# Optimization experiments

Measured on AMD Instinct MI355X. Metric: run time of the kernel, lower is better.

The kernel has to match this reference:

```python
import jax, jax.numpy as jnp
import numpy as np

DIM = 1024
D_STATE = 16
EXPAND = 2
D_CONV = 4
D_INNER = DIM * EXPAND          # 2048
DT_RANK = (DIM + 15) // 16      # ceil(dim/16) = 64
BATCH = 2
SEQ = 1024


def setup_inputs() -> dict:
    key = jax.random.key(0)
    ks = jax.random.split(key, 8)
    s = 0.02
    A = jnp.broadcast_to(jnp.arange(1, D_STATE + 1, dtype=jnp.float32), (D_INNER, D_STATE))
    return {
        "x": jax.random.normal(ks[0], (BATCH, SEQ, DIM), jnp.float32),
        "in_w": jax.random.normal(ks[1], (2 * D_INNER, DIM), jnp.float32) * s,
        "conv_w": jax.random.normal(ks[2], (D_INNER, 1, D_CONV), jnp.float32) * s,   # depthwise conv kernel (OIH)
        "conv_b": jnp.zeros((D_INNER,), jnp.float32),
        "xproj_w": jax.random.normal(ks[3], (DT_RANK + 2 * D_STATE, D_INNER), jnp.float32) * s,
        "dt_w": jax.random.normal(ks[4], (D_INNER, DT_RANK), jnp.float32) * s,
        "dt_b": jax.random.normal(ks[5], (D_INNER,), jnp.float32) * s,
        "A_log": jnp.log(A),
        "D": jnp.ones((D_INNER,), jnp.float32),
        "out_w": jax.random.normal(ks[6], (DIM, D_INNER), jnp.float32) * s,
    }


def _selective_scan(u, delta, A, B, C, D):
    # u: (b, d_in, l); delta: (b, l, d_in); A: (d_in, n); B, C: (b, l, n); D: (d_in,)
    dA = jnp.exp(jnp.einsum('bld,dn->lbdn', delta, A))          # (l, b, d_in, n)
    dBu = jnp.einsum('bld,bln,bdl->lbdn', delta, B, u)          # (l, b, d_in, n)
    Ct = jnp.transpose(C, (1, 0, 2))                            # (l, b, n)

    def step(carry, inp):
        a, bu, c = inp
        carry = a * carry + bu                                  # (b, d_in, n)
        y = jnp.einsum('bdn,bn->bd', carry, c)
        return carry, y

    x0 = jnp.zeros(dA.shape[1:], dA.dtype)
    _, ys = jax.lax.scan(step, x0, (dA, dBu, Ct))               # ys: (l, b, d_in)
    y = jnp.transpose(ys, (1, 2, 0))                            # (b, d_in, l)
    return y + u * D[:, None]


def reference(x, in_w, conv_w, conv_b, xproj_w, dt_w, dt_b, A_log, D, out_w):
    b, l, d = x.shape
    xr = x @ in_w.T                                             # (b, l, 2*d_in)
    xx, res = jnp.split(xr, 2, axis=-1)
    xx = jnp.transpose(xx, (0, 2, 1))                           # (b, d_in, l)
    # causal depthwise conv: left-pad d_conv-1 == torch pad=d_conv-1 then [:, :, :l]
    xx = jax.lax.conv_general_dilated(
        xx, conv_w, window_strides=(1,), padding=[(D_CONV - 1, 0)],
        dimension_numbers=('NCH', 'OIH', 'NCH'), feature_group_count=D_INNER
    ) + conv_b[None, :, None]
    xx = jax.nn.silu(xx)
    A = -jnp.exp(A_log)
    x_dbl = jnp.einsum('bdl,kd->blk', xx, xproj_w)              # (b, l, dt_rank + 2n)
    delta, B, C = jnp.split(x_dbl, [DT_RANK, DT_RANK + D_STATE], axis=-1)
    delta = jax.nn.softplus(delta @ dt_w.T + dt_b)              # (b, l, d_in)
    y = _selective_scan(xx, delta, A, B, C, D)                  # (b, d_in, l)
    y = y * jax.nn.silu(jnp.transpose(res, (0, 2, 1)))
    return jnp.transpose(y, (0, 2, 1)) @ out_w.T                # (b, l, dim)
```

## Files before the change

### kernel.cpp

```cpp
#include <hip/hip_runtime.h>
#include <hip/hip_bf16.h>
#include <stdint.h>

#define DIM      1024
#define D_STATE  16
#define D_CONV   4
#define D_INNER  2048
#define DT_RANK  64
#define BATCH    2
#define SEQ      1024
#define MROWS    (BATCH * SEQ)
#define NPROJ    (2 * D_INNER)
#define XDBL_K   (DT_RANK + 2 * D_STATE)

#define LC       16
#define NC       (SEQ / LC)
#define SLANES   (BATCH * D_INNER * D_STATE)

typedef __attribute__((ext_vector_type(8))) short short8;
typedef __attribute__((ext_vector_type(4))) float f32x4;
typedef unsigned short ushort_t;

__device__ __forceinline__ unsigned short f2bf(float f) {
    __hip_bfloat16 b = __float2bfloat16(f);
    return *reinterpret_cast<unsigned short*>(&b);
}
__device__ __forceinline__ float bf2f(unsigned short u) {
    __hip_bfloat16 b;
    *reinterpret_cast<unsigned short*>(&b) = u;
    return __bfloat162float(b);
}

__device__ __forceinline__ void gload_lds16(const unsigned short* g, unsigned short* l) {
    __builtin_amdgcn_global_load_lds(
        (const __attribute__((address_space(1))) void*)g,
        (__attribute__((address_space(3))) void*)l,
        16, 0, 0);
}

#define SG0 524288
#define SG1 1048576
#define SG2 65536
#define SG3 524288
#define SPLIT_GRANULES (SG0 + SG1 + SG2 + SG3)

__global__ __launch_bounds__(256) void split_all(
    const float* __restrict__ x,   const float* __restrict__ in_w,
    const float* __restrict__ xpw, const float* __restrict__ ow,
    ushort_t* __restrict__ xh,   ushort_t* __restrict__ xl,
    ushort_t* __restrict__ iwh,  ushort_t* __restrict__ xph,
    ushort_t* __restrict__ owh)
{
    int g = blockIdx.x * 256 + threadIdx.x;
    const float* src; int K, rows_src; ushort_t *dh, *dl; bool lo;
    if (g < SG0)               { src = x;    K = 1024; rows_src = 2048; dh = xh;  dl = xl; lo = true;  }
    else if ((g -= SG0) < SG1) { src = in_w; K = 1024; rows_src = 4096; dh = iwh; dl = 0;  lo = false; }
    else if ((g -= SG1) < SG2) { src = xpw;  K = 2048; rows_src = 96;   dh = xph; dl = 0;  lo = false; }
    else                       { g -= SG2;   src = ow; K = 2048; rows_src = 1024; dh = owh; dl = 0; lo = false; }

    const int kq = K >> 2;
    const int r = g / kq;
    const int k4 = (g - r * kq) << 2;
    float4 v = make_float4(0.f, 0.f, 0.f, 0.f);
    if (r < rows_src)
        v = *reinterpret_cast<const float4*>(src + (size_t)r * K + k4);
    const unsigned short h0 = f2bf(v.x), h1 = f2bf(v.y), h2 = f2bf(v.z), h3 = f2bf(v.w);
    *reinterpret_cast<ushort4*>(dh + (size_t)r * K + k4) = make_ushort4(h0, h1, h2, h3);
    if (lo) {
        const unsigned short l0 = f2bf(v.x - bf2f(h0)), l1 = f2bf(v.y - bf2f(h1));
        const unsigned short l2 = f2bf(v.z - bf2f(h2)), l3 = f2bf(v.w - bf2f(h3));
        *reinterpret_cast<ushort4*>(dl + (size_t)r * K + k4) = make_ushort4(l0, l1, l2, l3);
    }
}

__device__ __forceinline__ short8 frag_ld(const unsigned short* base, int row, int slot) {
    const char* p = reinterpret_cast<const char*>(base) +
                    row * 128 + (((slot ^ (row & 7)) & 7) << 4);
    return *reinterpret_cast<const short8*>(p);
}

template <int EPI>
__global__ __launch_bounds__(256) void gemm_bf2(
    const ushort_t* __restrict__ Ahg, const ushort_t* __restrict__ Alg, int lda,
    const ushort_t* __restrict__ Bhg, int ldb,
    float* __restrict__ C, int ldc, size_t czstride,
    const float* __restrict__ bias, int kLen)
{
    __shared__ ushort_t Ahs[128 * 64];
    __shared__ ushort_t Als[128 * 64];
    __shared__ ushort_t Bhs[128 * 64];

    const int tid = threadIdx.x;
    const int lane = tid & 63;
    const int w = tid >> 6;
    const int wr = w >> 1, wc = w & 1;
    const int fr = lane & 15, fg = lane >> 4;
    const int m0 = blockIdx.y * 128;
    const int n0 = blockIdx.x * 128;
    const int kOff = blockIdx.z * kLen;
    Ahg += kOff; Alg += kOff; Bhg += kOff;
    C += (size_t)blockIdx.z * czstride;

    f32x4 zero = {0.f, 0.f, 0.f, 0.f};
    f32x4 acc[4][4];
#pragma unroll
    for (int i = 0; i < 4; ++i)
#pragma unroll
        for (int j = 0; j < 4; ++j) acc[i][j] = zero;

    for (int k0 = 0; k0 < kLen; k0 += 64) {
#pragma unroll
        for (int it = 0; it < 4; ++it) {
            const int f = it * 256 + tid;
            const int row = f >> 3;
            const int gc = ((f & 7) ^ (row & 7)) << 3;
            const size_t ga = (size_t)(m0 + row) * lda + k0 + gc;
            const size_t gb = (size_t)(n0 + row) * ldb + k0 + gc;
            gload_lds16(Ahg + ga, &Ahs[f * 8]);
            gload_lds16(Alg + ga, &Als[f * 8]);
            gload_lds16(Bhg + gb, &Bhs[f * 8]);
        }
        __syncthreads();

#pragma unroll
        for (int kk = 0; kk < 2; ++kk) {
            short8 ah[4], bh[4], al[4];
#pragma unroll
            for (int i = 0; i < 4; ++i) {
                ah[i] = frag_ld(Ahs, wr * 64 + i * 16 + fr, kk * 4 + fg);
                bh[i] = frag_ld(Bhs, wc * 64 + i * 16 + fr, kk * 4 + fg);
            }
#pragma unroll
            for (int i = 0; i < 4; ++i)
#pragma unroll
                for (int j = 0; j < 4; ++j)
                    acc[i][j] = __builtin_amdgcn_mfma_f32_16x16x32_bf16(
                        ah[i], bh[j], acc[i][j], 0, 0, 0);
#pragma unroll
            for (int i = 0; i < 4; ++i)
                al[i] = frag_ld(Als, wr * 64 + i * 16 + fr, kk * 4 + fg);
#pragma unroll
            for (int i = 0; i < 4; ++i)
#pragma unroll
                for (int j = 0; j < 4; ++j)
                    acc[i][j] = __builtin_amdgcn_mfma_f32_16x16x32_bf16(
                        al[i], bh[j], acc[i][j], 0, 0, 0);
        }
        __syncthreads();
    }

#pragma unroll
    for (int i = 0; i < 4; ++i) {
        const int mrow = m0 + wr * 64 + i * 16 + fg * 4;
#pragma unroll
        for (int j = 0; j < 4; ++j) {
            const int col = n0 + wc * 64 + j * 16 + fr;
#pragma unroll
            for (int r = 0; r < 4; ++r) {
                float v = acc[i][j][r];
                if constexpr (EPI == 1) {
                    v += bias[col];
                    v = (v > 20.f) ? v : log1pf(__expf(v));
                }
                C[(size_t)(mrow + r) * ldc + col] = v;
            }
        }
    }
}

#define DTC 64
#define DTR 64
__global__ __launch_bounds__(256) void dt_softplus(
    const float* __restrict__ XDBL, const float* __restrict__ dtw,
    const float* __restrict__ dtb, float* __restrict__ DELTA)
{
    __shared__ float X[DTR][68];

    const int tid = threadIdx.x;
    const int lane = tid & 63;
    const int wv = tid >> 6;
    const int d = blockIdx.x * DTC + lane;
    const int m0 = blockIdx.y * DTR;

#pragma unroll
    for (int i = 0; i < 4; ++i) {
        const int g = tid + i * 256;
        const int r = g >> 4;
        const int q4 = (g & 15) << 2;
        const float4 v = *reinterpret_cast<const float4*>(
            XDBL + (size_t)(m0 + r) * XDBL_K + q4);
        *reinterpret_cast<float4*>(&X[r][q4]) = v;
    }

    float wreg[DT_RANK];
#pragma unroll
    for (int k4 = 0; k4 < DT_RANK / 4; ++k4) {
        const float4 v = *reinterpret_cast<const float4*>(
            dtw + (size_t)d * DT_RANK + k4 * 4);
        wreg[k4 * 4 + 0] = v.x;
        wreg[k4 * 4 + 1] = v.y;
        wreg[k4 * 4 + 2] = v.z;
        wreg[k4 * 4 + 3] = v.w;
    }
    const float bias = dtb[d];
    __syncthreads();

#pragma unroll
    for (int r = 0; r < DTR / 4; ++r) {
        const int rl = wv * (DTR / 4) + r;
        float a0 = bias, a1 = 0.f, a2 = 0.f, a3 = 0.f;
#pragma unroll
        for (int k = 0; k < DT_RANK; k += 4) {
            const float4 xv = *reinterpret_cast<const float4*>(&X[rl][k]);
            a0 = fmaf(xv.x, wreg[k + 0], a0);
            a1 = fmaf(xv.y, wreg[k + 1], a1);
            a2 = fmaf(xv.z, wreg[k + 2], a2);
            a3 = fmaf(xv.w, wreg[k + 3], a3);
        }
        float acc = (a0 + a1) + (a2 + a3);
        acc = (acc > 20.f) ? acc : log1pf(__expf(acc));
        DELTA[(size_t)(m0 + rl) * D_INNER + d] = acc;
    }
}

__global__ __launch_bounds__(256) void conv_silu(
    const float* __restrict__ XR, const float* __restrict__ cw,
    const float* __restrict__ cb, ushort_t* __restrict__ Uh,
    ushort_t* __restrict__ Ul)
{
    const int idx = blockIdx.x * 256 + threadIdx.x;
    const int d = idx & (D_INNER - 1);
    const int m = idx >> 11;
    const int l = m & (SEQ - 1);

    float acc = cb[d];
#pragma unroll
    for (int j = 0; j < D_CONV; ++j) {
        const int ll = l - (D_CONV - 1) + j;
        if (ll >= 0)
            acc = fmaf(XR[(size_t)(m - (D_CONV - 1) + j) * NPROJ + d],
                       cw[d * D_CONV + j], acc);
    }
    const float s = acc / (1.f + __expf(-acc));
    const unsigned short h = f2bf(s);
    Uh[idx] = h;
    Ul[idx] = f2bf(s - bf2f(h));
}

__global__ __launch_bounds__(256) void scan_phase1(
    const float* __restrict__ DELTA, const ushort_t* __restrict__ Uh,
    const ushort_t* __restrict__ Ul, const float* __restrict__ XDBL,
    const float* __restrict__ A_log, float* __restrict__ P,
    float* __restrict__ HL)
{
    const int tid = threadIdx.x;
    const int d = blockIdx.x * 256 + tid;
    const int c = blockIdx.y;
    const int b = blockIdx.z;

    float a[16];
#pragma unroll
    for (int q = 0; q < 4; ++q) {
        const float4 v = *reinterpret_cast<const float4*>(A_log + (size_t)d * 16 + q * 4);
        a[q * 4 + 0] = -__expf(v.x);
        a[q * 4 + 1] = -__expf(v.y);
        a[q * 4 + 2] = -__expf(v.z);
        a[q * 4 + 3] = -__expf(v.w);
    }
    float h[16];
#pragma unroll
    for (int n = 0; n < 16; ++n) h[n] = 0.f;
    float sd = 0.f;
    const size_t base = (size_t)b * SEQ + (size_t)c * LC;

#pragma unroll 4
    for (int t = 0; t < LC; ++t) {
        const size_t m = base + t;
        const float delta = DELTA[m * D_INNER + d];
        const float u = bf2f(Uh[m * D_INNER + d]) + bf2f(Ul[m * D_INNER + d]);
        const float du = delta * u;
        const float* xb = XDBL + m * XDBL_K + DT_RANK;
        float bv[16];
#pragma unroll
        for (int n = 0; n < 16; ++n) bv[n] = xb[n];
        sd += delta;
#pragma unroll
        for (int n = 0; n < 16; ++n) {
            const float dA = __expf(delta * a[n]);
            h[n] = fmaf(dA, h[n], du * bv[n]);
        }
    }

    const size_t idx = (size_t)c * SLANES + ((size_t)b * D_INNER + d) * 16;
#pragma unroll
    for (int q = 0; q < 4; ++q) {
        float4 pv, hv;
        pv.x = __expf(a[q * 4 + 0] * sd);
        pv.y = __expf(a[q * 4 + 1] * sd);
        pv.z = __expf(a[q * 4 + 2] * sd);
        pv.w = __expf(a[q * 4 + 3] * sd);
        hv.x = h[q * 4 + 0]; hv.y = h[q * 4 + 1];
        hv.z = h[q * 4 + 2]; hv.w = h[q * 4 + 3];
        *reinterpret_cast<float4*>(&P[idx + q * 4]) = pv;
        *reinterpret_cast<float4*>(&HL[idx + q * 4]) = hv;
    }
}

__global__ __launch_bounds__(256) void scan_phase2(
    float* __restrict__ P, const float* __restrict__ HL)
{
    const int t = blockIdx.x * 256 + threadIdx.x;
    float h = 0.f;
#pragma unroll 8
    for (int c = 0; c < NC; ++c) {
        const size_t idx = (size_t)c * SLANES + t;
        const float p = P[idx];
        const float hl = HL[idx];
        P[idx] = h;
        h = fmaf(p, h, hl);
    }
}

__global__ __launch_bounds__(256) void scan_phase3(
    const float* __restrict__ DELTA, const ushort_t* __restrict__ Uh,
    const ushort_t* __restrict__ Ul, const float* __restrict__ XDBL,
    const float* __restrict__ XR, const float* __restrict__ A_log,
    const float* __restrict__ Dp, const float* __restrict__ H0,
    ushort_t* __restrict__ Yh, ushort_t* __restrict__ Yl)
{
    const int tid = threadIdx.x;
    const int d = blockIdx.x * 256 + tid;
    const int c = blockIdx.y;
    const int b = blockIdx.z;

    float a[16];
#pragma unroll
    for (int q = 0; q < 4; ++q) {
        const float4 v = *reinterpret_cast<const float4*>(A_log + (size_t)d * 16 + q * 4);
        a[q * 4 + 0] = -__expf(v.x);
        a[q * 4 + 1] = -__expf(v.y);
        a[q * 4 + 2] = -__expf(v.z);
        a[q * 4 + 3] = -__expf(v.w);
    }
    const float Dd = Dp[d];

    float h[16];
    const size_t idx0 = (size_t)c * SLANES + ((size_t)b * D_INNER + d) * 16;
#pragma unroll
    for (int q = 0; q < 4; ++q) {
        const float4 v = *reinterpret_cast<const float4*>(&H0[idx0 + q * 4]);
        h[q * 4 + 0] = v.x; h[q * 4 + 1] = v.y;
        h[q * 4 + 2] = v.z; h[q * 4 + 3] = v.w;
    }
    const size_t base = (size_t)b * SEQ + (size_t)c * LC;

#pragma unroll 4
    for (int t = 0; t < LC; ++t) {
        const size_t m = base + t;
        const float delta = DELTA[m * D_INNER + d];
        const float u = bf2f(Uh[m * D_INNER + d]) + bf2f(Ul[m * D_INNER + d]);
        const float du = delta * u;
        const float* xb = XDBL + m * XDBL_K + DT_RANK;
        float bv[16], cv[16];
#pragma unroll
        for (int n = 0; n < 16; ++n) bv[n] = xb[n];
#pragma unroll
        for (int n = 0; n < 16; ++n) cv[n] = xb[16 + n];

        float y0 = 0.f, y1 = 0.f, y2 = 0.f, y3 = 0.f;
#pragma unroll
        for (int n = 0; n < 4; ++n) {
            const float dA0 = __expf(delta * a[n]);
            const float dA1 = __expf(delta * a[n + 4]);
            const float dA2 = __expf(delta * a[n + 8]);
            const float dA3 = __expf(delta * a[n + 12]);
            h[n]      = fmaf(dA0, h[n],      du * bv[n]);
            h[n + 4]  = fmaf(dA1, h[n + 4],  du * bv[n + 4]);
            h[n + 8]  = fmaf(dA2, h[n + 8],  du * bv[n + 8]);
            h[n + 12] = fmaf(dA3, h[n + 12], du * bv[n + 12]);
            y0 = fmaf(h[n],      cv[n],      y0);
            y1 = fmaf(h[n + 4],  cv[n + 4],  y1);
            y2 = fmaf(h[n + 8],  cv[n + 8],  y2);
            y3 = fmaf(h[n + 12], cv[n + 12], y3);
        }
        const float y = (y0 + y1) + (y2 + y3) + u * Dd;
        const float r = XR[m * NPROJ + D_INNER + d];
        const float sr = r / (1.f + __expf(-r));
        const float yg = y * sr;
        const unsigned short hh = f2bf(yg);
        Yh[m * D_INNER + d] = hh;
        Yl[m * D_INNER + d] = f2bf(yg - bf2f(hh));
    }
}

__global__ __launch_bounds__(256) void reduce_xdbl(
    const float* __restrict__ PP, float* __restrict__ XDBL)
{
    const int t = blockIdx.x * 256 + threadIdx.x;
    const int m = t / XDBL_K;
    const int n = t - m * XDBL_K;
    float s = 0.f;
#pragma unroll
    for (int z = 0; z < 16; ++z)
        s += PP[(size_t)z * MROWS * 128 + (size_t)m * 128 + n];
    XDBL[t] = s;
}

__global__ __launch_bounds__(256) void reduce_out(
    const float* __restrict__ OP, float* __restrict__ out)
{
    const int t = blockIdx.x * 256 + threadIdx.x;
    float4 s = *reinterpret_cast<const float4*>(OP + (size_t)t * 4);
#pragma unroll
    for (int z = 1; z < 4; ++z) {
        const float4 v = *reinterpret_cast<const float4*>(
            OP + (size_t)z * MROWS * DIM + (size_t)t * 4);
        s.x += v.x; s.y += v.y; s.z += v.z; s.w += v.w;
    }
    *reinterpret_cast<float4*>(out + (size_t)t * 4) = s;
}

extern "C" void kernel_launch(void* const* d_in, const int* in_sizes, int n_in,
                              void* d_out, int out_size, void* d_ws, size_t ws_size,
                              hipStream_t stream)
{
    const float* x       = (const float*)d_in[0];
    const float* in_w    = (const float*)d_in[1];
    const float* conv_w  = (const float*)d_in[2];
    const float* conv_b  = (const float*)d_in[3];
    const float* xproj_w = (const float*)d_in[4];
    const float* dt_w    = (const float*)d_in[5];
    const float* dt_b    = (const float*)d_in[6];
    const float* A_log   = (const float*)d_in[7];
    const float* Dp      = (const float*)d_in[8];
    const float* out_w   = (const float*)d_in[9];
    float* out = (float*)d_out;

    const size_t MF = 1024 * 1024;
    float* WF    = (float*)d_ws;
    float* XR    = WF;
    float* DELTA = WF + 8 * MF;
    float* XDBL  = WF + 12 * MF;
    float* PP    = WF + 13 * MF;
    float* P     = WF + 13 * MF;
    float* HL    = WF + 17 * MF;
    float* OP    = WF;

    ushort_t* UB  = (ushort_t*)(WF + 21 * MF);
    ushort_t* xh  = UB;
    ushort_t* xl  = UB + 2 * MF;
    ushort_t* iwh = UB + 4 * MF;
    ushort_t* Uh  = UB;
    ushort_t* Ul  = UB + 4 * MF;
    ushort_t* Yh  = UB + 8 * MF;
    ushort_t* Yl  = (ushort_t*)(WF + 17 * MF);
    ushort_t* xph = UB + 12 * MF;
    ushort_t* owh = xph + 256 * 1024;

    const dim3 blk(256);

    split_all<<<SPLIT_GRANULES / 256, blk, 0, stream>>>(
        x, in_w, xproj_w, out_w, xh, xl, iwh, xph, owh);

    gemm_bf2<0><<<dim3(NPROJ / 128, MROWS / 128, 1), blk, 0, stream>>>(
        xh, xl, DIM, iwh, DIM, XR, NPROJ, 0, nullptr, DIM);

    conv_silu<<<(MROWS * D_INNER) / 256, blk, 0, stream>>>(XR, conv_w, conv_b, Uh, Ul);

    gemm_bf2<0><<<dim3(1, MROWS / 128, 16), blk, 0, stream>>>(
        Uh, Ul, D_INNER, xph, D_INNER, PP, 128, (size_t)MROWS * 128, nullptr, D_INNER / 16);
    reduce_xdbl<<<(MROWS * XDBL_K) / 256, blk, 0, stream>>>(PP, XDBL);

    dt_softplus<<<dim3(D_INNER / DTC, MROWS / DTR), blk, 0, stream>>>(
        XDBL, dt_w, dt_b, DELTA);

    scan_phase1<<<dim3(D_INNER / 256, NC, BATCH), blk, 0, stream>>>(
        DELTA, Uh, Ul, XDBL, A_log, P, HL);
    scan_phase2<<<SLANES / 256, blk, 0, stream>>>(P, HL);
    scan_phase3<<<dim3(D_INNER / 256, NC, BATCH), blk, 0, stream>>>(
        DELTA, Uh, Ul, XDBL, XR, A_log, Dp, P, Yh, Yl);

    gemm_bf2<0><<<dim3(DIM / 128, MROWS / 128, 4), blk, 0, stream>>>(
        Yh, Yl, D_INNER, owh, D_INNER, OP, DIM, (size_t)MROWS * DIM, nullptr, D_INNER / 4);
    reduce_out<<<(MROWS * DIM / 4) / 256, blk, 0, stream>>>(OP, out);
}
```

Before: 213.3 us.

## Fuse silu(res) into in-proj GEMM epilogue and retile out-proj split-K

The in-projection GEMM now writes the x half as a compact fp32 buffer and applies SiLU to the residual half in its epilogue, storing it as bf16. The scan's final phase then reads that bf16 gate instead of recomputing SiLU from fp32. The GEMM gains a BN template parameter, and the output projection uses 64-wide N tiles with 2-way split-K instead of 4, which halves the partial-sum traffic in reduce_out. In exchange, the gate is rounded to bf16 precision, and the smaller tiles give less data reuse per block.

After: 209.4 us, median of 2. No clear change (-1.8%).

```diff
diff --git a/kernel.cpp b/kernel.cpp
--- a/kernel.cpp
+++ b/kernel.cpp
@@ -79,16 +79,17 @@
     return *reinterpret_cast<const short8*>(p);
 }
 
-template <int EPI>
+template <int EPI, int BN>
 __global__ __launch_bounds__(256) void gemm_bf2(
     const ushort_t* __restrict__ Ahg, const ushort_t* __restrict__ Alg, int lda,
     const ushort_t* __restrict__ Bhg, int ldb,
     float* __restrict__ C, int ldc, size_t czstride,
-    const float* __restrict__ bias, int kLen)
-{
+    ushort_t* __restrict__ SR, int kLen)
+{
+    constexpr int NJ = BN / 32;
     __shared__ ushort_t Ahs[128 * 64];
     __shared__ ushort_t Als[128 * 64];
-    __shared__ ushort_t Bhs[128 * 64];
+    __shared__ ushort_t Bhs[BN * 64];
 
     const int tid = threadIdx.x;
     const int lane = tid & 63;
@@ -96,17 +97,17 @@
     const int wr = w >> 1, wc = w & 1;
     const int fr = lane & 15, fg = lane >> 4;
     const int m0 = blockIdx.y * 128;
-    const int n0 = blockIdx.x * 128;
+    const int n0 = blockIdx.x * BN;
     const int kOff = blockIdx.z * kLen;
     Ahg += kOff; Alg += kOff; Bhg += kOff;
     C += (size_t)blockIdx.z * czstride;
 
     f32x4 zero = {0.f, 0.f, 0.f, 0.f};
-    f32x4 acc[4][4];
+    f32x4 acc[4][NJ];
 #pragma unroll
     for (int i = 0; i < 4; ++i)
 #pragma unroll
-        for (int j = 0; j < 4; ++j) acc[i][j] = zero;
+        for (int j = 0; j < NJ; ++j) acc[i][j] = zero;
 
     for (int k0 = 0; k0 < kLen; k0 += 64) {
 #pragma unroll
@@ -115,25 +116,32 @@
             const int row = f >> 3;
             const int gc = ((f & 7) ^ (row & 7)) << 3;
             const size_t ga = (size_t)(m0 + row) * lda + k0 + gc;
-            const size_t gb = (size_t)(n0 + row) * ldb + k0 + gc;
             gload_lds16(Ahg + ga, &Ahs[f * 8]);
             gload_lds16(Alg + ga, &Als[f * 8]);
+        }
+#pragma unroll
+        for (int it = 0; it < BN / 32; ++it) {
+            const int f = it * 256 + tid;
+            const int row = f >> 3;
+            const int gc = ((f & 7) ^ (row & 7)) << 3;
+            const size_t gb = (size_t)(n0 + row) * ldb + k0 + gc;
             gload_lds16(Bhg + gb, &Bhs[f * 8]);
         }
         __syncthreads();
 
 #pragma unroll
         for (int kk = 0; kk < 2; ++kk) {
-            short8 ah[4], bh[4], al[4];
-#pragma unroll
-            for (int i = 0; i < 4; ++i) {
+            short8 ah[4], bh[NJ], al[4];
+#pragma unroll
+            for (int i = 0; i < 4; ++i)
                 ah[i] = frag_ld(Ahs, wr * 64 + i * 16 + fr, kk * 4 + fg);
-                bh[i] = frag_ld(Bhs, wc * 64 + i * 16 + fr, kk * 4 + fg);
-            }
+#pragma unroll
+            for (int i = 0; i < NJ; ++i)
+                bh[i] = frag_ld(Bhs, wc * (BN / 2) + i * 16 + fr, kk * 4 + fg);
 #pragma unroll
             for (int i = 0; i < 4; ++i)
 #pragma unroll
-                for (int j = 0; j < 4; ++j)
+                for (int j = 0; j < NJ; ++j)
                     acc[i][j] = __builtin_amdgcn_mfma_f32_16x16x32_bf16(
                         ah[i], bh[j], acc[i][j], 0, 0, 0);
 #pragma unroll
@@ -142,7 +150,7 @@
 #pragma unroll
             for (int i = 0; i < 4; ++i)
 #pragma unroll
-                for (int j = 0; j < 4; ++j)
+                for (int j = 0; j < NJ; ++j)
                     acc[i][j] = __builtin_amdgcn_mfma_f32_16x16x32_bf16(
                         al[i], bh[j], acc[i][j], 0, 0, 0);
         }
@@ -153,16 +161,21 @@
     for (int i = 0; i < 4; ++i) {
         const int mrow = m0 + wr * 64 + i * 16 + fg * 4;
 #pragma unroll
-        for (int j = 0; j < 4; ++j) {
-            const int col = n0 + wc * 64 + j * 16 + fr;
+        for (int j = 0; j < NJ; ++j) {
+            const int col = n0 + wc * (BN / 2) + j * 16 + fr;
 #pragma unroll
             for (int r = 0; r < 4; ++r) {
                 float v = acc[i][j][r];
-                if constexpr (EPI == 1) {
-                    v += bias[col];
-                    v = (v > 20.f) ? v : log1pf(__expf(v));
+                if constexpr (EPI == 2) {
+                    if (n0 < D_INNER) {
+                        C[(size_t)(mrow + r) * D_INNER + col] = v;
+                    } else {
+                        const float sv = v / (1.f + __expf(-v));
+                        SR[(size_t)(mrow + r) * D_INNER + col - D_INNER] = f2bf(sv);
+                    }
+                } else {
+                    C[(size_t)(mrow + r) * ldc + col] = v;
                 }
-                C[(size_t)(mrow + r) * ldc + col] = v;
             }
         }
     }
@@ -224,7 +237,7 @@
 }
 
 __global__ __launch_bounds__(256) void conv_silu(
-    const float* __restrict__ XR, const float* __restrict__ cw,
+    const float* __restrict__ XX, const float* __restrict__ cw,
     const float* __restrict__ cb, ushort_t* __restrict__ Uh,
     ushort_t* __restrict__ Ul)
 {
@@ -238,7 +251,7 @@
     for (int j = 0; j < D_CONV; ++j) {
         const int ll = l - (D_CONV - 1) + j;
         if (ll >= 0)
-            acc = fmaf(XR[(size_t)(m - (D_CONV - 1) + j) * NPROJ + d],
+            acc = fmaf(XX[(size_t)(m - (D_CONV - 1) + j) * D_INNER + d],
                        cw[d * D_CONV + j], acc);
     }
     const float s = acc / (1.f + __expf(-acc));
@@ -324,7 +337,7 @@
 __global__ __launch_bounds__(256) void scan_phase3(
     const float* __restrict__ DELTA, const ushort_t* __restrict__ Uh,
     const ushort_t* __restrict__ Ul, const float* __restrict__ XDBL,
-    const float* __restrict__ XR, const float* __restrict__ A_log,
+    const ushort_t* __restrict__ SR, const float* __restrict__ A_log,
     const float* __restrict__ Dp, const float* __restrict__ H0,
     ushort_t* __restrict__ Yh, ushort_t* __restrict__ Yl)
 {
@@ -384,8 +397,7 @@
             y3 = fmaf(h[n + 12], cv[n + 12], y3);
         }
         const float y = (y0 + y1) + (y2 + y3) + u * Dd;
-        const float r = XR[m * NPROJ + D_INNER + d];
-        const float sr = r / (1.f + __expf(-r));
+        const float sr = bf2f(SR[m * D_INNER + d]);
         const float yg = y * sr;
         const unsigned short hh = f2bf(yg);
         Yh[m * D_INNER + d] = hh;
@@ -410,14 +422,11 @@
     const float* __restrict__ OP, float* __restrict__ out)
 {
     const int t = blockIdx.x * 256 + threadIdx.x;
-    float4 s = *reinterpret_cast<const float4*>(OP + (size_t)t * 4);
-#pragma unroll
-    for (int z = 1; z < 4; ++z) {
-        const float4 v = *reinterpret_cast<const float4*>(
-            OP + (size_t)z * MROWS * DIM + (size_t)t * 4);
-        s.x += v.x; s.y += v.y; s.z += v.z; s.w += v.w;
-    }
-    *reinterpret_cast<float4*>(out + (size_t)t * 4) = s;
+    const float4 a = *reinterpret_cast<const float4*>(OP + (size_t)t * 4);
+    const float4 b = *reinterpret_cast<const float4*>(OP + (size_t)MROWS * DIM + (size_t)t * 4);
+    float4 r;
+    r.x = a.x + b.x; r.y = a.y + b.y; r.z = a.z + b.z; r.w = a.w + b.w;
+    *reinterpret_cast<float4*>(out + (size_t)t * 4) = r;
 }
 
 extern "C" void kernel_launch(void* const* d_in, const int* in_sizes, int n_in,
@@ -438,7 +447,8 @@
 
     const size_t MF = 1024 * 1024;
     float* WF    = (float*)d_ws;
-    float* XR    = WF;
+    float* XX    = WF;
+    ushort_t* SRb = (ushort_t*)(WF + 4 * MF);
     float* DELTA = WF + 8 * MF;
     float* XDBL  = WF + 12 * MF;
     float* PP    = WF + 13 * MF;
@@ -462,12 +472,12 @@
     split_all<<<SPLIT_GRANULES / 256, blk, 0, stream>>>(
         x, in_w, xproj_w, out_w, xh, xl, iwh, xph, owh);
 
-    gemm_bf2<0><<<dim3(NPROJ / 128, MROWS / 128, 1), blk, 0, stream>>>(
-        xh, xl, DIM, iwh, DIM, XR, NPROJ, 0, nullptr, DIM);
-
-    conv_silu<<<(MROWS * D_INNER) / 256, blk, 0, stream>>>(XR, conv_w, conv_b, Uh, Ul);
-
-    gemm_bf2<0><<<dim3(1, MROWS / 128, 16), blk, 0, stream>>>(
+    gemm_bf2<2, 128><<<dim3(NPROJ / 128, MROWS / 128, 1), blk, 0, stream>>>(
+        xh, xl, DIM, iwh, DIM, XX, D_INNER, 0, SRb, DIM);
+
+    conv_silu<<<(MROWS * D_INNER) / 256, blk, 0, stream>>>(XX, conv_w, conv_b, Uh, Ul);
+
+    gemm_bf2<0, 128><<<dim3(1, MROWS / 128, 16), blk, 0, stream>>>(
         Uh, Ul, D_INNER, xph, D_INNER, PP, 128, (size_t)MROWS * 128, nullptr, D_INNER / 16);
     reduce_xdbl<<<(MROWS * XDBL_K) / 256, blk, 0, stream>>>(PP, XDBL);
 
@@ -478,9 +488,9 @@
         DELTA, Uh, Ul, XDBL, A_log, P, HL);
     scan_phase2<<<SLANES / 256, blk, 0, stream>>>(P, HL);
     scan_phase3<<<dim3(D_INNER / 256, NC, BATCH), blk, 0, stream>>>(
-        DELTA, Uh, Ul, XDBL, XR, A_log, Dp, P, Yh, Yl);
-
-    gemm_bf2<0><<<dim3(DIM / 128, MROWS / 128, 4), blk, 0, stream>>>(
-        Yh, Yl, D_INNER, owh, D_INNER, OP, DIM, (size_t)MROWS * DIM, nullptr, D_INNER / 4);
+        DELTA, Uh, Ul, XDBL, SRb, A_log, Dp, P, Yh, Yl);
+
+    gemm_bf2<0, 64><<<dim3(DIM / 64, MROWS / 128, 2), blk, 0, stream>>>(
+        Yh, Yl, D_INNER, owh, D_INNER, OP, DIM, (size_t)MROWS * DIM, nullptr, D_INNER / 2);
     reduce_out<<<(MROWS * DIM / 4) / 256, blk, 0, stream>>>(OP, out);
 }
```
